# Kernel optimization log

Measured on AMD Instinct MI355X. Metric: run time of the kernel, lower is better.

The kernel has to match this reference:

```python
import jax, jax.numpy as jnp
import numpy as np

B, T, D, H = 2, 4096, 1024, 16
DK, DV, C = 64, 128, 64  # head_k_dim, head_v_dim, chunk size


def setup_inputs() -> dict:
    key = jax.random.key(0)
    ks = jax.random.split(key, 7)
    std = 0.02
    return {
        "x": jax.random.normal(ks[0], (B, T, D), jnp.float32),
        "Wq": jax.random.normal(ks[1], (D, D), jnp.float32) * std,
        "Wk": jax.random.normal(ks[2], (D, D), jnp.float32) * std,
        "Wv": jax.random.normal(ks[3], (D, 2 * D), jnp.float32) * std,
        "Wg": jax.random.normal(ks[4], (D, 2 * D), jnp.float32) * std,
        "Wo": jax.random.normal(ks[5], (2 * D, D), jnp.float32) * std,
        "g_norm_w": jnp.ones((DV,), jnp.float32),
    }


def _rope(q, k):  # q,k: [B,T,H,DK], neox-style rotate-half rotary
    dk = q.shape[-1]
    inv = 1.0 / (10000.0 ** (jnp.arange(0, dk, 2, dtype=jnp.float32) / dk))
    t = jnp.arange(q.shape[1], dtype=jnp.float32)
    f = t[:, None] * inv[None, :]                      # [T, dk/2]
    cos = jnp.cos(f)[None, :, None, :]
    sin = jnp.sin(f)[None, :, None, :]
    def rot(x):
        x1, x2 = jnp.split(x, 2, axis=-1)
        return jnp.concatenate([x1 * cos - x2 * sin, x1 * sin + x2 * cos], -1)
    return rot(q), rot(k)


def reference(x, Wq, Wk, Wv, Wg, Wo, g_norm_w):
    b, t, _ = x.shape
    nc = t // C
    q = (x @ Wq).reshape(b, t, H, DK)
    k = (x @ Wk).reshape(b, t, H, DK)
    v = (x @ Wv).reshape(b, t, H, DV)
    g = (x @ Wg).reshape(b, t, H, DV)
    q, k = _rope(q, k)
    q = q * (DK ** -0.5)

    # per-head retention decay: gamma_h = 1 - 2^(-5-h)
    gamma = 1.0 - jnp.exp2(-5.0 - jnp.arange(H, dtype=jnp.float32))  # [H]
    i = jnp.arange(C, dtype=jnp.float32)
    dq = gamma[:, None] ** (i + 1.0)          # [H,C] cross-chunk decay on q
    dkv = gamma[:, None] ** (C - 1.0 - i)     # [H,C] decay of k into state
    rel = i[:, None] - i[None, :]
    Dmat = jnp.where(rel >= 0, gamma[:, None, None] ** jnp.maximum(rel, 0.0), 0.0)  # [H,C,C]
    gC = gamma ** C

    to_chunks = lambda a: a.reshape(b, nc, C, H, a.shape[-1]).transpose(1, 0, 3, 2, 4)
    qc, kc, vc = to_chunks(q), to_chunks(k), to_chunks(v)  # [NC,B,H,C,d]

    def step(S, inp):
        qi, ki, vi = inp
        o_inter = jnp.einsum('bhcd,bhde->bhce', qi * dq[None, :, :, None], S)
        A = jnp.einsum('bhid,bhjd->bhij', qi, ki) * Dmat[None]
        o_intra = jnp.einsum('bhij,bhje->bhie', A, vi)
        S = gC[None, :, None, None] * S + jnp.einsum('bhjd,bhje->bhde', ki * dkv[None, :, :, None], vi)
        return S, o_inter + o_intra

    S0 = jnp.zeros((b, H, DK, DV), x.dtype)
    _, o = jax.lax.scan(step, S0, (qc, kc, vc))            # [NC,B,H,C,DV]
    o = o.transpose(1, 0, 3, 2, 4).reshape(b, t, H, DV)

    # fused per-head RMSNorm + swish gate
    rms = o * jax.lax.rsqrt(jnp.mean(o * o, axis=-1, keepdims=True) + 1e-5) * g_norm_w
    o = rms * (g * jax.nn.sigmoid(g))
    return o.reshape(b, t, H * DV) @ Wo
```

## Files before the change

kernel.cpp:

```cpp
#include <hip/hip_runtime.h>
#include <stdint.h>
#include <type_traits>

typedef unsigned short u16;
typedef __attribute__((ext_vector_type(8))) short short8;
typedef __attribute__((ext_vector_type(4))) float f32x4;

#define MFMA16(a,b,c) __builtin_amdgcn_mfma_f32_16x16x32_bf16(a,b,c,0,0,0)

__device__ __forceinline__ u16 f2bf(float f){
  uint32_t u = __builtin_bit_cast(uint32_t, f);
  u += 0x7FFFu + ((u>>16)&1u);
  return (u16)(u>>16);
}
__device__ __forceinline__ float bf2f(u16 h){
  uint32_t u = ((uint32_t)h)<<16;
  return __builtin_bit_cast(float, u);
}

__global__ __launch_bounds__(256) void prep(const float* __restrict__ x, u16* __restrict__ xb,
    const float* __restrict__ Wq, const float* __restrict__ Wk, const float* __restrict__ Wv,
    const float* __restrict__ Wg, const float* __restrict__ Wo,
    u16* __restrict__ WcatT, u16* __restrict__ WoT){
  int bid = blockIdx.x;
  if (bid < 8192){
    int i = (bid*256 + threadIdx.x)*4;
    float4 v = *(const float4*)&x[i];
    uint2 u;
    u.x = (uint32_t)f2bf(v.x) | ((uint32_t)f2bf(v.y)<<16);
    u.y = (uint32_t)f2bf(v.z) | ((uint32_t)f2bf(v.w)<<16);
    *(uint2*)&xb[i] = u;
    return;
  }
  bid -= 8192;
  const float* src; u16* dst; int R, Cc, tc, tr;
  if (bid < 1024){        src=Wq; dst=WcatT;             R=1024; Cc=1024; int b=bid;      tc=(b&31)*32; tr=(b>>5)*32; }
  else if (bid < 2048){   src=Wk; dst=WcatT+1024*1024;   R=1024; Cc=1024; int b=bid-1024; tc=(b&31)*32; tr=(b>>5)*32; }
  else if (bid < 4096){   src=Wv; dst=WcatT+2048*1024;   R=1024; Cc=2048; int b=bid-2048; tc=(b&63)*32; tr=(b>>6)*32; }
  else if (bid < 6144){   src=Wg; dst=WcatT+4096*1024;   R=1024; Cc=2048; int b=bid-4096; tc=(b&63)*32; tr=(b>>6)*32; }
  else {                  src=Wo; dst=WoT;               R=2048; Cc=1024; int b=bid-6144; tc=(b&31)*32; tr=(b>>5)*32; }
  __shared__ float tile[32][33];
  int lr = threadIdx.x>>5, lc = threadIdx.x&31;
  #pragma unroll
  for (int p=0;p<4;p++)
    tile[lr+p*8][lc] = src[(size_t)(tr+lr+p*8)*Cc + tc + lc];
  __syncthreads();
  #pragma unroll
  for (int p=0;p<4;p++)
    dst[(size_t)(tc+lr+p*8)*R + tr + lc] = f2bf(tile[lc][lr+p*8]);
}

__global__ __launch_bounds__(512,1) void gemm1_256(const u16* __restrict__ A,
    const u16* __restrict__ BT, u16* __restrict__ C){
  __shared__ u16 L[2*32768];
  const int flat = blockIdx.y*24 + blockIdx.x;
  const int xcd  = flat & 7, loc = flat >> 3;
  const int bm   = xcd*4 + (loc & 3);
  const int bn   = loc >> 2;
  const int t = threadIdx.x;
  const int w = t>>6, l = t&63;
  const int wm = w>>2, wn = w&3;
  const int lr = l&15, lg = l>>4;
  const int srow = t>>2;
  const int gsw = ((t&3) - (t>>3)) & 3;
  const size_t aoff = (size_t)(bm*256 + srow)*1024 + gsw*8;
  const size_t boff = (size_t)(bn*256 + srow)*1024 + gsw*8;
  const int sdo = t*8;

  u16 *cur = L, *oth = L + 32768;

  auto STAGE = [&](u16* buf, int k0){
    #pragma unroll
    for (int ks=0; ks<2; ++ks){
      __builtin_amdgcn_global_load_lds(&A[aoff + k0 + ks*32],                     buf + ks*8192 + sdo,               16,0,0);
      __builtin_amdgcn_global_load_lds(&A[aoff + (size_t)128*1024 + k0 + ks*32],  buf + ks*8192 + sdo + 4096,        16,0,0);
      __builtin_amdgcn_global_load_lds(&BT[boff + k0 + ks*32],                    buf + 16384 + ks*8192 + sdo,        16,0,0);
      __builtin_amdgcn_global_load_lds(&BT[boff + (size_t)128*1024 + k0 + ks*32], buf + 16384 + ks*8192 + sdo + 4096, 16,0,0);
    }
  };
  auto LDA = [&](const u16* base, int row)->short8 {
    return *(const short8*)(base + row*32 + (((lg + (row>>1))&3)<<3));
  };

  f32x4 acc[8][4];
  #pragma unroll
  for (int m=0;m<8;m++)
    #pragma unroll
    for (int n=0;n<4;n++) acc[m][n] = (f32x4){0.f,0.f,0.f,0.f};

  STAGE(cur, 0);
  asm volatile("s_waitcnt vmcnt(0)" ::: "memory");
  __builtin_amdgcn_s_barrier();
  short8 f0A[8], f0B[4], f1A[8], f1B[4];
  #pragma unroll
  for (int m=0;m<8;m++) f0A[m] = LDA(cur, wm*128 + m*16 + lr);
  #pragma unroll
  for (int n=0;n<4;n++) f0B[n] = LDA(cur + 16384, wn*64 + n*16 + lr);

  for (int kt=0; kt<16; ++kt){
    #pragma unroll
    for (int m=0;m<8;m++) f1A[m] = LDA(cur + 8192, wm*128 + m*16 + lr);
    #pragma unroll
    for (int n=0;n<4;n++) f1B[n] = LDA(cur + 16384 + 8192, wn*64 + n*16 + lr);
    if (kt+1 < 16) STAGE(oth, (kt+1)*64);
    __builtin_amdgcn_s_setprio(1);
    #pragma unroll
    for (int m=0;m<8;m++)
      #pragma unroll
      for (int n=0;n<4;n++)
        acc[m][n] = MFMA16(f0A[m], f0B[n], acc[m][n]);
    __builtin_amdgcn_s_setprio(0);
    asm volatile("s_waitcnt lgkmcnt(0)" ::: "memory");
    __builtin_amdgcn_sched_barrier(0);
    asm volatile("s_waitcnt vmcnt(0)" ::: "memory");
    __builtin_amdgcn_s_barrier();
    __builtin_amdgcn_sched_barrier(0);
    if (kt+1 < 16){
      #pragma unroll
      for (int m=0;m<8;m++) f0A[m] = LDA(oth, wm*128 + m*16 + lr);
      #pragma unroll
      for (int n=0;n<4;n++) f0B[n] = LDA(oth + 16384, wn*64 + n*16 + lr);
    }
    __builtin_amdgcn_s_setprio(1);
    #pragma unroll
    for (int m=0;m<8;m++)
      #pragma unroll
      for (int n=0;n<4;n++)
        acc[m][n] = MFMA16(f1A[m], f1B[n], acc[m][n]);
    __builtin_amdgcn_s_setprio(0);
    { u16* tp=cur; cur=oth; oth=tp; }
  }

  __syncthreads();
  const bool qk = (bn < 8);
  const float qscale = (bn < 4) ? 0.125f : 1.0f;
  #pragma unroll
  for (int s=0;s<4;++s){
    if (wm == (s>>1)){
      #pragma unroll
      for (int mm=0;mm<4;++mm){
        const int m = (s&1)*4 + mm;
        if (qk){
          #pragma unroll
          for (int n=0;n<2;n++){
            float inv = exp2f((float)(n*16+lr) * (-13.287712379549449f/32.0f));
            #pragma unroll
            for (int r=0;r<4;r++){
              int grow = bm*256 + wm*128 + m*16 + lg*4 + r;
              float f = (float)(grow & 4095) * inv;
              float sn, cs; __sincosf(f, &sn, &cs);
              float x1 = acc[m][n][r], x2 = acc[m][n+2][r];
              int lrow = mm*16 + lg*4 + r;
              L[lrow*264 + wn*64 + n*16 + lr]     = f2bf((x1*cs - x2*sn)*qscale);
              L[lrow*264 + wn*64 + (n+2)*16 + lr] = f2bf((x1*sn + x2*cs)*qscale);
            }
          }
        } else {
          #pragma unroll
          for (int n=0;n<4;n++)
            #pragma unroll
            for (int r=0;r<4;r++)
              L[(mm*16+lg*4+r)*264 + wn*64 + n*16 + lr] = f2bf(acc[m][n][r]);
        }
      }
    }
    __syncthreads();
    #pragma unroll
    for (int p=0;p<4;p++){
      int idx = p*512 + t;
      int row = idx>>5, gr = idx&31;
      *(short8*)&C[(size_t)(bm*256 + s*64 + row)*6144 + bn*256 + gr*8] =
        *(const short8*)&L[row*264 + gr*8];
    }
    __syncthreads();
  }
}

__global__ __launch_bounds__(256) void gemm2_nt(const u16* __restrict__ A,
    const u16* __restrict__ BT, float* __restrict__ C, int M, int N, int K){
  __shared__ u16 L[3*8192];
  const int flat = blockIdx.y*gridDim.x + blockIdx.x;
  const int xcd  = flat & 7, loc = flat >> 3;
  const int bm   = xcd*8 + (loc & 7);
  const int bn   = loc >> 3;
  const int t = threadIdx.x;
  const int w = t>>6, l = t&63;
  const int wr = (w>>1)*64, wc = (w&1)*64;
  const int lr = l&15, lg = l>>4;
  const int srow = t>>2;
  const int gsw  = ((t&3) - (t>>3)) & 3;
  const int scol = gsw*8;
  const size_t aoff = (size_t)(bm*128 + srow)*K + scol;
  const size_t boff = (size_t)(bn*128 + srow)*K + scol;
  const int sdo = t*8;

  u16 *a0 = L,          *b0 = L + 4096;
  u16 *a1 = L + 8192,   *b1 = L + 12288;
  u16 *a2 = L + 16384,  *b2 = L + 20480;

  auto STAGE = [&](u16* la, u16* lb, int k0){
    __builtin_amdgcn_global_load_lds(&A[aoff + k0],                 la + sdo,        16, 0, 0);
    __builtin_amdgcn_global_load_lds(&A[aoff + (size_t)64*K + k0],  la + sdo + 2048, 16, 0, 0);
    __builtin_amdgcn_global_load_lds(&BT[boff + k0],                lb + sdo,        16, 0, 0);
    __builtin_amdgcn_global_load_lds(&BT[boff + (size_t)64*K + k0], lb + sdo + 2048, 16, 0, 0);
  };
  auto LDR = [&](const u16* base, int row)->short8 {
    return *(const short8*)(base + row*32 + (((lg + (row>>1))&3)<<3));
  };

  f32x4 acc[4][4];
  for (int m=0;m<4;m++) for (int n=0;n<4;n++) acc[m][n] = (f32x4){0.f,0.f,0.f,0.f};

  const int NT = K >> 5;
  STAGE(a0, b0, 0);
  STAGE(a1, b1, 32);
  asm volatile("s_waitcnt vmcnt(4)" ::: "memory");
  __builtin_amdgcn_s_barrier();
  short8 af01[2], af23[2], bfr[4], bfrn[4];
  #pragma unroll
  for (int m=0;m<2;m++) af01[m] = LDR(a0, wr + m*16 + lr);
  #pragma unroll
  for (int n=0;n<4;n++) bfr[n] = LDR(b0, wc + n*16 + lr);

  for (int kt=0; kt<NT; ++kt){
    #pragma unroll
    for (int m=0;m<2;m++) af23[m] = LDR(a0, wr + (m+2)*16 + lr);
    if (kt+2 < NT) STAGE(a2, b2, (kt+2)*32);
    __builtin_amdgcn_s_setprio(1);
    #pragma unroll
    for (int m=0;m<2;m++)
      #pragma unroll
      for (int n=0;n<4;n++)
        acc[m][n] = MFMA16(af01[m], bfr[n], acc[m][n]);
    __builtin_amdgcn_s_setprio(0);
    asm volatile("s_waitcnt lgkmcnt(0)" ::: "memory");
    __builtin_amdgcn_sched_barrier(0);
    if (kt < NT-2) asm volatile("s_waitcnt vmcnt(4)" ::: "memory");
    else           asm volatile("s_waitcnt vmcnt(0)" ::: "memory");
    __builtin_amdgcn_s_barrier();
    __builtin_amdgcn_sched_barrier(0);
    if (kt+1 < NT){
      #pragma unroll
      for (int m=0;m<2;m++) af01[m] = LDR(a1, wr + m*16 + lr);
      #pragma unroll
      for (int n=0;n<4;n++) bfrn[n] = LDR(b1, wc + n*16 + lr);
    }
    __builtin_amdgcn_s_setprio(1);
    #pragma unroll
    for (int m=0;m<2;m++)
      #pragma unroll
      for (int n=0;n<4;n++)
        acc[m+2][n] = MFMA16(af23[m], bfr[n], acc[m+2][n]);
    __builtin_amdgcn_s_setprio(0);
    if (kt+1 < NT){
      #pragma unroll
      for (int n=0;n<4;n++) bfr[n] = bfrn[n];
    }
    { u16* tp=a0; a0=a1; a1=a2; a2=tp; }
    { u16* tp=b0; b0=b1; b1=b2; b2=tp; }
  }

  #pragma unroll
  for (int m=0;m<4;m++)
    #pragma unroll
    for (int n=0;n<4;n++){
    int row = bm*128 + wr + m*16 + lg*4;
    int col = bn*128 + wc + n*16 + lr;
    #pragma unroll
    for (int r=0;r<4;r++)
      C[(size_t)(row+r)*N + col] = acc[m][n][r];
  }
}

__global__ __launch_bounds__(256) void retention_r1(const u16* __restrict__ qkvg,
    u16* __restrict__ o, u16* __restrict__ states){
  int bid = blockIdx.x;
  int c = bid & 63, h = (bid>>6)&15, b = bid>>10;
  int t = threadIdx.x, w = t>>6, l = t&63, lr = l&15, lg = l>>4;
  __shared__ u16 SH[17280];
  __shared__ float pw[72];
  u16* kT    = SH;
  u16* vT    = SH + 4096;
  u16* A_lds = SH + 12288;
  float log2g = log2f(1.0f - exp2f(-5.0f - (float)h));
  if (t < 65) pw[t] = exp2f(log2g*(float)t);
  const size_t rowbase = (size_t)(b*4096 + c*64);
  __syncthreads();

  {
    int rp = t>>3, cg = t&7;
    int r0 = rp*2;
    short8 k0v = *(const short8*)&qkvg[(rowbase+r0  )*6144 + 1024 + h*64 + cg*8];
    short8 k1v = *(const short8*)&qkvg[(rowbase+r0+1)*6144 + 1024 + h*64 + cg*8];
    float d0 = pw[63-r0], d1 = pw[62-r0];
    #pragma unroll
    for (int j=0;j<8;j++){
      int d = cg*8+j;
      uint32_t pk = (uint32_t)f2bf(bf2f((u16)k0v[j])*d0) | ((uint32_t)f2bf(bf2f((u16)k1v[j])*d1)<<16);
      *(uint32_t*)&kT[d*64 + (((r0>>3) ^ (d>>3))<<3) + (r0&7)] = pk;
    }
    #pragma unroll
    for (int p=0;p<2;p++){
      int it = t + p*256;
      int vrp = it>>4, vcg = it&15;
      int vr0 = vrp*2;
      short8 v0 = *(const short8*)&qkvg[(rowbase+vr0  )*6144 + 2048 + h*128 + vcg*8];
      short8 v1 = *(const short8*)&qkvg[(rowbase+vr0+1)*6144 + 2048 + h*128 + vcg*8];
      #pragma unroll
      for (int j=0;j<8;j++){
        int e = vcg*8+j;
        uint32_t pv = (uint32_t)(u16)v0[j] | ((uint32_t)(u16)v1[j]<<16);
        *(uint32_t*)&vT[e*64 + (((vr0>>3) ^ ((e>>3)&7))<<3) + (vr0&7)] = pv;
      }
    }
  }

  f32x4 z4 = {0.f,0.f,0.f,0.f};
  f32x4 accA[4] = {z4,z4,z4,z4};
  #pragma unroll
  for (int ks=0;ks<2;ks++){
    short8 aq = *(const short8*)&qkvg[(rowbase + w*16+lr)*6144 + h*64 + ks*32 + lg*8];
    #pragma unroll
    for (int n=0;n<4;n++){
      short8 bk = *(const short8*)&qkvg[(rowbase + n*16+lr)*6144 + 1024 + h*64 + ks*32 + lg*8];
      accA[n] = MFMA16(aq, bk, accA[n]);
    }
  }
  #pragma unroll
  for (int n=0;n<4;n++)
    #pragma unroll
    for (int r=0;r<4;r++){
    int i = w*16 + lg*4 + r, j = n*16 + lr;
    float v = (i>=j) ? accA[n][r]*pw[i-j] : 0.0f;
    A_lds[i*72 + j] = f2bf(v);
  }
  __syncthreads();

  f32x4 accO[8], accS[8];
  #pragma unroll
  for (int n=0;n<8;n++){ accO[n]=z4; accS[n]=z4; }
  #pragma unroll
  for (int ks=0;ks<2;ks++){
    int rk = w*16+lr;
    short8 aA = *(const short8*)&A_lds[rk*72 + ks*32+lg*8];
    short8 aK = *(const short8*)&kT[rk*64 + (((ks*4+lg) ^ (rk>>3))<<3)];
    #pragma unroll
    for (int n=0;n<8;n++){
      int e2 = n*16+lr;
      short8 bv = *(const short8*)&vT[e2*64 + (((ks*4+lg) ^ ((e2>>3)&7))<<3)];
      accO[n] = MFMA16(aA, bv, accO[n]);
      accS[n] = MFMA16(aK, bv, accS[n]);
    }
  }

  __syncthreads();
  u16* oB = SH;
  u16* sB = SH + 8448;
  #pragma unroll
  for (int n=0;n<8;n++)
    #pragma unroll
    for (int r=0;r<4;r++){
    int i = w*16 + lg*4 + r, e = n*16 + lr;
    oB[i*132 + e] = f2bf(accO[n][r]);
    sB[e*68 + i]  = f2bf(accS[n][r]);
  }
  __syncthreads();
  const size_t ob = rowbase*2048 + h*128;
  const size_t sb = ((size_t)(b*16+h)*64 + c)*8192;
  {
    int orow = t>>2, ocol = (t&3)*32;
    #pragma unroll
    for (int q=0;q<4;q++)
      *(short8*)&o[ob + (size_t)orow*2048 + ocol + q*8] = *(const short8*)&oB[orow*132 + ocol + q*8];
    int se = t>>1, sd = (t&1)*32;
    #pragma unroll
    for (int q=0;q<4;q++)
      *(short8*)&states[sb + (size_t)se*64 + sd + q*8] = *(const short8*)&sB[se*68 + sd + q*8];
  }
}

__global__ __launch_bounds__(256) void retention_r2(const u16* __restrict__ qkvg,
    const u16* __restrict__ states, u16* __restrict__ o){
  int bid = blockIdx.x;
  int xq = bid & 7, qq = bid >> 3;
  int bh = xq*4 + (qq & 3);
  int vblk = qq >> 2;
  int h = bh & 15, b = bh >> 4;
  int t = threadIdx.x, w = t>>6, l = t&63, lr = l&15, lg = l>>4;
  int e0 = vblk*16;
  float log2g = log2f(1.0f - exp2f(-5.0f - (float)h));
  float gC = exp2f(64.0f*log2g);
  float dqv[4];
  #pragma unroll
  for (int r=0;r<4;r++) dqv[r] = exp2f(log2g*(float)(w*16 + lg*4 + r + 1));
  float st[16];
  #pragma unroll
  for (int i=0;i<16;i++) st[i]=0.f;
  const size_t sbase = ((size_t)(b*16+h)*64)*8192 + (size_t)(e0+lr)*64 + lg*8;
  const size_t qb = (size_t)(b*4096)*6144 + h*64 + (size_t)(w*16+lr)*6144 + lg*8;
  const size_t obh = (size_t)(b*4096)*2048 + h*128 + e0 + lr;
  short8 nsc0 = *(const short8*)&states[sbase];
  short8 nsc1 = *(const short8*)&states[sbase + 32];
  short8 naq0 = *(const short8*)&qkvg[qb];
  short8 naq1 = *(const short8*)&qkvg[qb + 32];
  for (int c=0;c<64;c++){
    short8 sc0 = nsc0, sc1 = nsc1, aq0 = naq0, aq1 = naq1;
    if (c < 63){
      nsc0 = *(const short8*)&states[sbase + (size_t)(c+1)*8192];
      nsc1 = *(const short8*)&states[sbase + (size_t)(c+1)*8192 + 32];
      naq0 = *(const short8*)&qkvg[qb + (size_t)(c+1)*64*6144];
      naq1 = *(const short8*)&qkvg[qb + (size_t)(c+1)*64*6144 + 32];
    }
    f32x4 acc = {0.f,0.f,0.f,0.f};
    short8 bs0, bs1;
    #pragma unroll
    for (int dd=0;dd<8;dd++) bs0[dd] = (short)f2bf(st[dd]);
    #pragma unroll
    for (int dd=0;dd<8;dd++) bs1[dd] = (short)f2bf(st[dd+8]);
    acc = MFMA16(aq0, bs0, acc);
    acc = MFMA16(aq1, bs1, acc);
    #pragma unroll
    for (int r=0;r<4;r++){
      int i = w*16 + lg*4 + r;
      size_t oi = obh + (size_t)(c*64 + i)*2048;
      o[oi] = f2bf(bf2f(o[oi]) + dqv[r]*acc[r]);
    }
    #pragma unroll
    for (int i2=0;i2<8;i2++) st[i2]   = gC*st[i2]   + bf2f((u16)sc0[i2]);
    #pragma unroll
    for (int i2=0;i2<8;i2++) st[i2+8] = gC*st[i2+8] + bf2f((u16)sc1[i2]);
  }
}

__global__ __launch_bounds__(256) void norm_gate(const u16* __restrict__ o,
    const u16* __restrict__ qkvg, const float* __restrict__ gnw, u16* __restrict__ og){
  int g16 = threadIdx.x >> 4;
  int l16 = threadIdx.x & 15;
  int rowh = blockIdx.x*16 + g16;
  int row = rowh >> 4, h = rowh & 15;
  short8 vv = *(const short8*)(o + (size_t)row*2048 + h*128 + l16*8);
  float v[8];
  float ss = 0.f;
  #pragma unroll
  for (int j=0;j<8;j++){ v[j] = bf2f((u16)vv[j]); ss += v[j]*v[j]; }
  #pragma unroll
  for (int off=8; off; off>>=1) ss += __shfl_xor(ss, off);
  float rs = rsqrtf(ss*(1.0f/128.0f) + 1e-5f);
  short8 gg = *(const short8*)(qkvg + (size_t)row*6144 + 4096 + h*128 + l16*8);
  float4 w0 = *(const float4*)&gnw[l16*8];
  float4 w1 = *(const float4*)&gnw[l16*8 + 4];
  float wv[8] = {w0.x,w0.y,w0.z,w0.w,w1.x,w1.y,w1.z,w1.w};
  short8 res;
  #pragma unroll
  for (int j=0;j<8;j++){
    float gj = bf2f((u16)gg[j]);
    float rj = v[j]*rs*wv[j] * (gj/(1.f+expf(-gj)));
    res[j] = (short)f2bf(rj);
  }
  *(short8*)(og + (size_t)row*2048 + h*128 + l16*8) = res;
}

extern "C" void kernel_launch(void* const* d_in, const int* in_sizes, int n_in,
                              void* d_out, int out_size, void* d_ws, size_t ws_size,
                              hipStream_t stream){
  const float* x   = (const float*)d_in[0];
  const float* Wq  = (const float*)d_in[1];
  const float* Wk  = (const float*)d_in[2];
  const float* Wv  = (const float*)d_in[3];
  const float* Wg  = (const float*)d_in[4];
  const float* Wo  = (const float*)d_in[5];
  const float* gnw = (const float*)d_in[6];
  float* out = (float*)d_out;

  const size_t NEED = 171966464ull;
  if (ws_size < NEED) return;

  char* base = (char*)d_ws;
  u16* qkvg  = (u16*)(base);
  u16* obuf  = (u16*)(base + 100663296);
  u16* WoT   = (u16*)(base + 134217728);
  u16* xb    = (u16*)(base + 138412032);
  u16* WcatT = (u16*)(base + 155189248);
  u16* stt   = (u16*)(base + 138412032);
  u16* og    = (u16*)(base + 138412032);

  prep<<<16384,256,0,stream>>>(x, xb, Wq, Wk, Wv, Wg, Wo, WcatT, WoT);
  gemm1_256<<<dim3(24,32),512,0,stream>>>(xb, WcatT, qkvg);
  retention_r1<<<2048,256,0,stream>>>(qkvg, obuf, stt);
  retention_r2<<<256,256,0,stream>>>(qkvg, stt, obuf);
  norm_gate<<<8192,256,0,stream>>>(obuf, qkvg, gnw, og);
  gemm2_nt<<<dim3(8,64),256,0,stream>>>(og, WoT, out, 8192, 1024, 2048);
}
```

Before: 284.4 us.

## Split GEMM main loop into four barrier-synchronized phases with finer-grained staging

Restructures the projection GEMM mainloop from two big MFMA blocks per k-tile into four phases, each computing half the M fragments on one k-slice. The global-to-LDS staging is split into separate A and B pieces interleaved between phases, with partial vmcnt waits. Fragment registers shrink from 24 short8 to 12, which frees VGPRs. In exchange there are many more s_barriers per iteration, and the vmcnt accounting becomes more intricate, which risks stalls or races.

```diff
diff --git a/kernel.cpp b/kernel.cpp
--- a/kernel.cpp
+++ b/kernel.cpp
@@ -69,14 +69,13 @@
 
   u16 *cur = L, *oth = L + 32768;
 
-  auto STAGE = [&](u16* buf, int k0){
-    #pragma unroll
-    for (int ks=0; ks<2; ++ks){
-      __builtin_amdgcn_global_load_lds(&A[aoff + k0 + ks*32],                     buf + ks*8192 + sdo,               16,0,0);
-      __builtin_amdgcn_global_load_lds(&A[aoff + (size_t)128*1024 + k0 + ks*32],  buf + ks*8192 + sdo + 4096,        16,0,0);
-      __builtin_amdgcn_global_load_lds(&BT[boff + k0 + ks*32],                    buf + 16384 + ks*8192 + sdo,        16,0,0);
-      __builtin_amdgcn_global_load_lds(&BT[boff + (size_t)128*1024 + k0 + ks*32], buf + 16384 + ks*8192 + sdo + 4096, 16,0,0);
-    }
+  auto STG_A = [&](u16* buf, int k0, int ks){
+    __builtin_amdgcn_global_load_lds(&A[aoff + k0 + ks*32],                    buf + ks*8192 + sdo,        16,0,0);
+    __builtin_amdgcn_global_load_lds(&A[aoff + (size_t)128*1024 + k0 + ks*32], buf + ks*8192 + sdo + 4096, 16,0,0);
+  };
+  auto STG_B = [&](u16* buf, int k0, int ks){
+    __builtin_amdgcn_global_load_lds(&BT[boff + k0 + ks*32],                    buf + 16384 + ks*8192 + sdo,        16,0,0);
+    __builtin_amdgcn_global_load_lds(&BT[boff + (size_t)128*1024 + k0 + ks*32], buf + 16384 + ks*8192 + sdo + 4096, 16,0,0);
   };
   auto LDA = [&](const u16* base, int row)->short8 {
     return *(const short8*)(base + row*32 + (((lg + (row>>1))&3)<<3));
@@ -88,46 +87,86 @@
     #pragma unroll
     for (int n=0;n<4;n++) acc[m][n] = (f32x4){0.f,0.f,0.f,0.f};
 
-  STAGE(cur, 0);
-  asm volatile("s_waitcnt vmcnt(0)" ::: "memory");
+  STG_A(cur, 0, 0); STG_B(cur, 0, 0); STG_A(cur, 0, 1); STG_B(cur, 0, 1);
+  asm volatile("s_waitcnt vmcnt(4)" ::: "memory");
   __builtin_amdgcn_s_barrier();
-  short8 f0A[8], f0B[4], f1A[8], f1B[4];
-  #pragma unroll
-  for (int m=0;m<8;m++) f0A[m] = LDA(cur, wm*128 + m*16 + lr);
-  #pragma unroll
-  for (int n=0;n<4;n++) f0B[n] = LDA(cur + 16384, wn*64 + n*16 + lr);
+  __builtin_amdgcn_sched_barrier(0);
+
+  short8 afA[4], afB[4], bf[4];
 
   for (int kt=0; kt<16; ++kt){
-    #pragma unroll
-    for (int m=0;m<8;m++) f1A[m] = LDA(cur + 8192, wm*128 + m*16 + lr);
-    #pragma unroll
-    for (int n=0;n<4;n++) f1B[n] = LDA(cur + 16384 + 8192, wn*64 + n*16 + lr);
-    if (kt+1 < 16) STAGE(oth, (kt+1)*64);
+    const int nk0 = (kt+1)*64;
+    #pragma unroll
+    for (int m=0;m<4;m++) afA[m] = LDA(cur, wm*128 + m*16 + lr);
+    #pragma unroll
+    for (int n=0;n<4;n++) bf[n] = LDA(cur + 16384, wn*64 + n*16 + lr);
+    if (kt+1 < 16) STG_A(oth, nk0, 0);
+    __builtin_amdgcn_s_barrier();
+    __builtin_amdgcn_sched_barrier(0);
+    asm volatile("s_waitcnt lgkmcnt(0)" ::: "memory");
+    __builtin_amdgcn_sched_barrier(0);
     __builtin_amdgcn_s_setprio(1);
     #pragma unroll
-    for (int m=0;m<8;m++)
+    for (int m=0;m<4;m++)
       #pragma unroll
       for (int n=0;n<4;n++)
-        acc[m][n] = MFMA16(f0A[m], f0B[n], acc[m][n]);
+        acc[m][n] = MFMA16(afA[m], bf[n], acc[m][n]);
     __builtin_amdgcn_s_setprio(0);
+    __builtin_amdgcn_s_barrier();
+    __builtin_amdgcn_sched_barrier(0);
+    #pragma unroll
+    for (int m=0;m<4;m++) afB[m] = LDA(cur, wm*128 + (m+4)*16 + lr);
+    if (kt+1 < 16) STG_B(oth, nk0, 0);
+    if (kt < 15) asm volatile("s_waitcnt vmcnt(4)" ::: "memory");
+    else         asm volatile("s_waitcnt vmcnt(0)" ::: "memory");
+    __builtin_amdgcn_s_barrier();
+    __builtin_amdgcn_sched_barrier(0);
     asm volatile("s_waitcnt lgkmcnt(0)" ::: "memory");
     __builtin_amdgcn_sched_barrier(0);
-    asm volatile("s_waitcnt vmcnt(0)" ::: "memory");
-    __builtin_amdgcn_s_barrier();
-    __builtin_amdgcn_sched_barrier(0);
-    if (kt+1 < 16){
-      #pragma unroll
-      for (int m=0;m<8;m++) f0A[m] = LDA(oth, wm*128 + m*16 + lr);
-      #pragma unroll
-      for (int n=0;n<4;n++) f0B[n] = LDA(oth + 16384, wn*64 + n*16 + lr);
-    }
     __builtin_amdgcn_s_setprio(1);
     #pragma unroll
-    for (int m=0;m<8;m++)
+    for (int m=0;m<4;m++)
       #pragma unroll
       for (int n=0;n<4;n++)
-        acc[m][n] = MFMA16(f1A[m], f1B[n], acc[m][n]);
+        acc[m+4][n] = MFMA16(afB[m], bf[n], acc[m+4][n]);
     __builtin_amdgcn_s_setprio(0);
+    __builtin_amdgcn_s_barrier();
+    __builtin_amdgcn_sched_barrier(0);
+    #pragma unroll
+    for (int m=0;m<4;m++) afA[m] = LDA(cur + 8192, wm*128 + m*16 + lr);
+    #pragma unroll
+    for (int n=0;n<4;n++) bf[n] = LDA(cur + 16384 + 8192, wn*64 + n*16 + lr);
+    if (kt+1 < 16) STG_A(oth, nk0, 1);
+    __builtin_amdgcn_s_barrier();
+    __builtin_amdgcn_sched_barrier(0);
+    asm volatile("s_waitcnt lgkmcnt(0)" ::: "memory");
+    __builtin_amdgcn_sched_barrier(0);
+    __builtin_amdgcn_s_setprio(1);
+    #pragma unroll
+    for (int m=0;m<4;m++)
+      #pragma unroll
+      for (int n=0;n<4;n++)
+        acc[m][n] = MFMA16(afA[m], bf[n], acc[m][n]);
+    __builtin_amdgcn_s_setprio(0);
+    __builtin_amdgcn_s_barrier();
+    __builtin_amdgcn_sched_barrier(0);
+    #pragma unroll
+    for (int m=0;m<4;m++) afB[m] = LDA(cur + 8192, wm*128 + (m+4)*16 + lr);
+    if (kt+1 < 16) STG_B(oth, nk0, 1);
+    if (kt+1 < 16) asm volatile("s_waitcnt vmcnt(4)" ::: "memory");
+    __builtin_amdgcn_s_barrier();
+    __builtin_amdgcn_sched_barrier(0);
+    asm volatile("s_waitcnt lgkmcnt(0)" ::: "memory");
+    __builtin_amdgcn_sched_barrier(0);
+    __builtin_amdgcn_s_setprio(1);
+    #pragma unroll
+    for (int m=0;m<4;m++)
+      #pragma unroll
+      for (int n=0;n<4;n++)
+        acc[m+4][n] = MFMA16(afB[m], bf[n], acc[m+4][n]);
+    __builtin_amdgcn_s_setprio(0);
+    __builtin_amdgcn_s_barrier();
+    __builtin_amdgcn_sched_barrier(0);
     { u16* tp=cur; cur=oth; oth=tp; }
   }
 
```

Result: no change. 284.5 us (+0.0%).
